# Kernel tuning notes

Hardware: AMD Instinct MI355X
Metric: run time of the kernel (lower is better)

Reference implementation:

```python
import jax, jax.numpy as jnp
import numpy as np

B, C_ATT, C_VAL = 1, 64, 64
T, H, W = 40, 32, 32
HW = H * W
TOPK = 10
TEMP = 0.07
NEIGHBOR_RANGE = 24  # circle mode -> radius = 24 // 2
NON_MASK_LEN = 1     # first frame is not masked
NEG_INF = -1e30


def _spatial_neighbor_circle(h, w, neighbor_range):
    """Circle-mode spatial neighbor mask, (h*w, h*w) bool."""
    radius = neighbor_range // 2
    gy, gx = jnp.meshgrid(jnp.arange(h, dtype=jnp.float32),
                          jnp.arange(w, dtype=jnp.float32), indexing='ij')
    dy = gy[:, :, None, None] - gy[None, None, :, :]
    dx = gx[:, :, None, None] - gx[None, None, :, :]
    dist = jnp.sqrt(dy * dy + dx * dx)
    return (dist < radius).reshape(h * w, h * w)


def setup_inputs() -> dict:
    key0 = jax.random.key(0)
    k1, k2, k3 = jax.random.split(key0, 3)
    query = jax.random.normal(k1, (B, C_ATT, H, W), dtype=jnp.float32)
    key = jax.random.normal(k2, (B, C_ATT, T, H, W), dtype=jnp.float32)
    value = jax.random.normal(k3, (B, C_VAL, T, H, W), dtype=jnp.float32)
    mask = _spatial_neighbor_circle(H, W, NEIGHBOR_RANGE)  # (HW, HW) bool
    return {"query": query, "key": key, "value": value, "mask": mask}


def _l2_normalize(x, axis, eps=1e-12):
    # matches F.normalize(p=2): x / max(||x||, eps)
    n = jnp.sqrt(jnp.sum(x * x, axis=axis, keepdims=True))
    return x / jnp.maximum(n, eps)


def reference(query, key, value, mask):
    # normalize along channel dim
    q = _l2_normalize(query, axis=1).reshape(B, C_ATT, HW)          # (B,C,Q)
    k = _l2_normalize(key, axis=1).reshape(B, C_ATT, T * HW)        # (B,C,K)
    v = value.reshape(B, C_VAL, T * HW)                             # (B,Cv,K)

    # affinity over all keys vs all queries (chunking in the original is a
    # pure memory optimization; the math per query column is identical)
    aff = jnp.einsum('bck,bcq->bkq', k, q) / TEMP                   # (B,K,Q)

    # build full mask: first NON_MASK_LEN frames fully visible, remaining
    # frames restricted to the spatial-neighbor circle
    tiled = jnp.tile(mask, (T - NON_MASK_LEN, 1))                   # ((T-nm)*HW, Q)
    full_mask = jnp.concatenate(
        [jnp.ones((NON_MASK_LEN * HW, HW), dtype=bool), tiled], axis=0)  # (K,Q)
    aff = jnp.where(full_mask[None], aff, NEG_INF)

    # top-k over the key dimension, per query
    aff_qk = jnp.swapaxes(aff, 1, 2)                                # (B,Q,K)
    top_vals, top_idx = jax.lax.top_k(aff_qk, TOPK)                 # (B,Q,topk)
    weights = jax.nn.softmax(top_vals, axis=-1)                     # (B,Q,topk)

    # gather top-k values: (B,Cv,Q,topk)
    gathered = jnp.take_along_axis(v[:, :, None, :], top_idx[:, None, :, :], axis=3)
    out = jnp.einsum('bcqk,bqk->bcq', gathered, weights)            # (B,Cv,Q)
    return out.reshape(B, C_VAL, H, W)
```

## Files before the change

### kernel.cpp

```cpp
#include <hip/hip_runtime.h>
#include <hip/hip_bf16.h>
#include <float.h>

#define HWQ   1024
#define NK    40960
#define NCH   64
#define NTOP  10
#define NJOBS 82
#define NPART (NJOBS * NTOP)
#define R2    144
#define CAP   48
#define TSCALE 14.2857142857142857f
#define LOSCL  4.8828125e-4f

typedef _Float16 f16x8 __attribute__((ext_vector_type(8)));
typedef float    f32x4 __attribute__((ext_vector_type(4)));
typedef unsigned long long u64;
typedef unsigned int       u32;

__device__ inline float bf16bits_to_f32(unsigned short u) {
    union { u32 i; float f; } z; z.i = ((u32)u) << 16; return z.f;
}
__device__ inline unsigned short f32_to_bf16bits(float x) {
    __hip_bfloat16 b = __float2bfloat16(x);
    return *(unsigned short*)&b;
}

__device__ inline int sniff_fp32(const unsigned short* __restrict__ raw) {
    const int lane = threadIdx.x & 63;
    const int e = (raw[lane] >> 7) & 0xFF;
    const u64 m = __ballot(e < 100 || e > 133);
    return __popcll(m) > 16;
}

__device__ inline u64 pack_vi(float val, int kidx) {
    const u32 b = __float_as_uint(val);
    const u32 u = b ^ (u32)(((int)b >> 31) | (int)0x80000000);
    return ((u64)u << 16) | (u32)(0xFFFF - kidx);
}
__device__ inline float unpack_val(u64 p) {
    const u32 u = (u32)(p >> 16);
    const u32 b = u ^ (~((u32)((int)u >> 31)) | 0x80000000u);
    return __uint_as_float(b);
}
__device__ inline int unpack_idx(u64 p) { return 0xFFFF - (int)(p & 0xFFFF); }

__device__ inline void ins10(u64* v, u64 pk) {
#pragma unroll
    for (int j = NTOP - 1; j >= 1; --j) {
        const bool gj = pk > v[j];
        const bool gp = pk > v[j - 1];
        v[j] = gj ? (gp ? v[j - 1] : pk) : v[j];
    }
    if (pk > v[0]) v[0] = pk;
}

__global__ __launch_bounds__(64) void prep_all(
    const void* __restrict__ qin_, const void* __restrict__ kin_,
    const void* __restrict__ vin_,
    f16x8* __restrict__ kh, f16x8* __restrict__ kl,
    f16x8* __restrict__ qh, f16x8* __restrict__ ql,
    unsigned short* __restrict__ vt)
{
    const int isf  = sniff_fp32((const unsigned short*)kin_);
    const int bid  = blockIdx.x;
    const int lane = threadIdx.x;

    if (bid < NK / 64) {
        const int key = bid * 64 + lane;
        float kv[NCH];
        if (isf) {
            const float* p = (const float*)kin_;
#pragma unroll
            for (int c = 0; c < NCH; ++c) kv[c] = p[c * NK + key];
        } else {
            const __hip_bfloat16* p = (const __hip_bfloat16*)kin_;
#pragma unroll
            for (int c = 0; c < NCH; ++c) kv[c] = __bfloat162float(p[c * NK + key]);
        }
        float s = 0.f;
#pragma unroll
        for (int c = 0; c < NCH; ++c) s = fmaf(kv[c], kv[c], s);
        const float rn = 1.0f / fmaxf(sqrtf(s), 1e-12f);

        const int tb = (key >> 4) * 128 + (key & 15);
#pragma unroll
        for (int blk = 0; blk < 8; ++blk) {
            f16x8 h, l;
#pragma unroll
            for (int j = 0; j < 8; ++j) {
                const float x = kv[blk * 8 + j] * rn;
                const _Float16 hh = (_Float16)x;
                h[j] = hh;
                l[j] = (_Float16)((x - (float)hh) * 2048.0f);
            }
            kh[tb + blk * 16] = h;
            kl[tb + blk * 16] = l;
        }

        if (isf) {
            const float* p = (const float*)vin_;
#pragma unroll
            for (int c = 0; c < NCH; ++c)
                vt[(size_t)key * NCH + c] = f32_to_bf16bits(p[c * NK + key]);
        } else {
            const unsigned short* p = (const unsigned short*)vin_;
#pragma unroll
            for (int c = 0; c < NCH; ++c) vt[(size_t)key * NCH + c] = p[c * NK + key];
        }
    } else {
        const int q = (bid - NK / 64) * 64 + lane;
        float qv[NCH];
        if (isf) {
            const float* p = (const float*)qin_;
#pragma unroll
            for (int c = 0; c < NCH; ++c) qv[c] = p[c * HWQ + q];
        } else {
            const __hip_bfloat16* p = (const __hip_bfloat16*)qin_;
#pragma unroll
            for (int c = 0; c < NCH; ++c) qv[c] = __bfloat162float(p[c * HWQ + q]);
        }
        float s = 0.f;
#pragma unroll
        for (int c = 0; c < NCH; ++c) s = fmaf(qv[c], qv[c], s);
        const float rn = 1.0f / fmaxf(sqrtf(s), 1e-12f);

        const int tb = (q >> 4) * 128 + (q & 15);
#pragma unroll
        for (int blk = 0; blk < 8; ++blk) {
            f16x8 h, l;
#pragma unroll
            for (int j = 0; j < 8; ++j) {
                const float x = qv[blk * 8 + j] * rn;
                const _Float16 hh = (_Float16)x;
                h[j] = hh;
                l[j] = (_Float16)((x - (float)hh) * 2048.0f);
            }
            qh[tb + blk * 16] = h;
            ql[tb + blk * 16] = l;
        }
    }
}

__device__ inline void quad_merge_store(
    u64 (*sm)[16][NTOP], int lane, u64* out10)
{
    int p0 = 0, p1 = 0, p2 = 0, p3 = 0;
#pragma unroll
    for (int r = 0; r < NTOP; ++r) {
        const u64 h0 = sm[0][lane][p0], h1 = sm[1][lane][p1];
        const u64 h2 = sm[2][lane][p2], h3 = sm[3][lane][p3];
        u64 m = h0; int sel = 0;
        if (h1 > m) { m = h1; sel = 1; }
        if (h2 > m) { m = h2; sel = 2; }
        if (h3 > m) { m = h3; sel = 3; }
        out10[r] = m;
        p0 += (sel == 0); p1 += (sel == 1); p2 += (sel == 2); p3 += (sel == 3);
    }
}

__global__ __launch_bounds__(128) void attn_f0(
    const f16x8* __restrict__ kh, const f16x8* __restrict__ kl,
    const f16x8* __restrict__ qh, const f16x8* __restrict__ ql,
    u64* __restrict__ pv, float* __restrict__ th)
{
    __shared__ u64 sm[2][4][16][NTOP];

    const int tid  = threadIdx.x;
    const int w    = tid >> 6;
    const int lane = tid & 63;
    const int quad = lane >> 4;
    const int n    = lane & 15;

    const int t   = blockIdx.x * 2 + w;
    const int job = blockIdx.y;

    const int qb = t * 128 + n;
    const f16x8 bh0 = qh[qb + (0 + quad) * 16];
    const f16x8 bh1 = qh[qb + (4 + quad) * 16];
    const f16x8 bl0 = ql[qb + (0 + quad) * 16];
    const f16x8 bl1 = ql[qb + (4 + quad) * 16];

    u64 v[NTOP];
#pragma unroll
    for (int j = 0; j < NTOP; ++j) v[j] = 0ull;

    const int start = job * 16, end = start + 16;
    int base = start * 128 + n;
    f16x8 nah0 = kh[base + (0 + quad) * 16], nah1 = kh[base + (4 + quad) * 16];
    f16x8 nal0 = kl[base + (0 + quad) * 16], nal1 = kl[base + (4 + quad) * 16];

    for (int kt = start; kt < end; ++kt) {
        const f16x8 ah0 = nah0, ah1 = nah1, al0 = nal0, al1 = nal1;
        const int ktn = (kt + 1 < end) ? kt + 1 : kt;
        base = ktn * 128 + n;
        nah0 = kh[base + (0 + quad) * 16]; nah1 = kh[base + (4 + quad) * 16];
        nal0 = kl[base + (0 + quad) * 16]; nal1 = kl[base + (4 + quad) * 16];

        f32x4 accH = {0.f,0.f,0.f,0.f}, accL0 = {0.f,0.f,0.f,0.f}, accL1 = {0.f,0.f,0.f,0.f};
        accH  = __builtin_amdgcn_mfma_f32_16x16x32_f16(ah0, bh0, accH, 0, 0, 0);
        accH  = __builtin_amdgcn_mfma_f32_16x16x32_f16(ah1, bh1, accH, 0, 0, 0);
        accL0 = __builtin_amdgcn_mfma_f32_16x16x32_f16(ah0, bl0, accL0, 0, 0, 0);
        accL0 = __builtin_amdgcn_mfma_f32_16x16x32_f16(al0, bh0, accL0, 0, 0, 0);
        accL1 = __builtin_amdgcn_mfma_f32_16x16x32_f16(ah1, bl1, accL1, 0, 0, 0);
        accL1 = __builtin_amdgcn_mfma_f32_16x16x32_f16(al1, bh1, accL1, 0, 0, 0);

        const int key0 = kt * 16 + quad * 4;
#pragma unroll
        for (int r = 0; r < 4; ++r) {
            const float val = fmaf(accL0[r] + accL1[r], LOSCL, accH[r]);
            const u64 pk = pack_vi(val, key0 + r);
            if (pk > v[NTOP - 1]) ins10(v, pk);
        }
    }

#pragma unroll
    for (int j = 0; j < NTOP; ++j) sm[w][quad][n][j] = v[j];
    __syncthreads();

    if (lane < 16) {
        u64 out10[NTOP];
        quad_merge_store(sm[w], lane, out10);
        const int q = t * 16 + lane;
#pragma unroll
        for (int r = 0; r < NTOP; ++r) pv[(size_t)q * NPART + job * NTOP + r] = out10[r];
        th[q * 4 + job] = unpack_val(out10[9]);
    }
}

__global__ __launch_bounds__(128) void attn_masked(
    const f16x8* __restrict__ kh, const f16x8* __restrict__ kl,
    const f16x8* __restrict__ qh, const f16x8* __restrict__ ql,
    const float* __restrict__ th, u64* __restrict__ pv)
{
    __shared__ u64 cand[2][16][CAP];
    __shared__ int cnt[2][16];

    const int tid  = threadIdx.x;
    const int w    = tid >> 6;
    const int lane = tid & 63;
    const int quad = lane >> 4;
    const int n    = lane & 15;

    const int qy   = blockIdx.x;
    const int t    = qy * 2 + w;
    const int yy   = blockIdx.y;
    const int f    = (yy >> 1) + 1;
    const int half = yy & 1;
    const int qx   = (t & 1) * 16 + n;
    const int q    = t * 16 + n;

    if (tid < 32) cnt[tid >> 4][tid & 15] = 0;
    __syncthreads();

    const float theta = fmaxf(fmaxf(th[q * 4 + 0], th[q * 4 + 1]),
                              fmaxf(th[q * 4 + 2], th[q * 4 + 3]));

    const int qb = t * 128 + n;
    const f16x8 bh0 = qh[qb + (0 + quad) * 16];
    const f16x8 bh1 = qh[qb + (4 + quad) * 16];
    const f16x8 bl0 = ql[qb + (0 + quad) * 16];
    const f16x8 bl1 = ql[qb + (4 + quad) * 16];

    const int rlo  = (qy > 11) ? qy - 11 : 0;
    const int rhi  = (qy < 20) ? qy + 11 : 31;
    const int mid  = (rlo + rhi + 1) >> 1;
    const int row0 = half ? mid : rlo;
    const int row1 = half ? rhi + 1 : mid;
    const int start = f * 64 + 2 * row0;
    const int end   = f * 64 + 2 * row1;

    int base = start * 128 + n;
    f16x8 nah0 = kh[base + (0 + quad) * 16], nah1 = kh[base + (4 + quad) * 16];
    f16x8 nal0 = kl[base + (0 + quad) * 16], nal1 = kl[base + (4 + quad) * 16];

    for (int kt = start; kt < end; ++kt) {
        const f16x8 ah0 = nah0, ah1 = nah1, al0 = nal0, al1 = nal1;
        const int ktn = (kt + 1 < end) ? kt + 1 : kt;
        base = ktn * 128 + n;
        nah0 = kh[base + (0 + quad) * 16]; nah1 = kh[base + (4 + quad) * 16];
        nal0 = kl[base + (0 + quad) * 16]; nal1 = kl[base + (4 + quad) * 16];

        f32x4 accH = {0.f,0.f,0.f,0.f}, accL0 = {0.f,0.f,0.f,0.f}, accL1 = {0.f,0.f,0.f,0.f};
        accH  = __builtin_amdgcn_mfma_f32_16x16x32_f16(ah0, bh0, accH, 0, 0, 0);
        accH  = __builtin_amdgcn_mfma_f32_16x16x32_f16(ah1, bh1, accH, 0, 0, 0);
        accL0 = __builtin_amdgcn_mfma_f32_16x16x32_f16(ah0, bl0, accL0, 0, 0, 0);
        accL0 = __builtin_amdgcn_mfma_f32_16x16x32_f16(al0, bh0, accL0, 0, 0, 0);
        accL1 = __builtin_amdgcn_mfma_f32_16x16x32_f16(ah1, bl1, accL1, 0, 0, 0);
        accL1 = __builtin_amdgcn_mfma_f32_16x16x32_f16(al1, bh1, accL1, 0, 0, 0);

        const int ky   = (kt >> 1) & 31;
        const int dy   = ky - qy;
        const int rem  = R2 - dy * dy;
        const int d0   = (kt & 1) * 16 + quad * 4 - qx;
        const int key0 = kt * 16 + quad * 4;
#pragma unroll
        for (int r = 0; r < 4; ++r) {
            const float val = fmaf(accL0[r] + accL1[r], LOSCL, accH[r]);
            const int dx = d0 + r;
            if (val > theta && dx * dx < rem) {
                const int pos = atomicAdd(&cnt[w][n], 1);
                if (pos < CAP) cand[w][n][pos] = pack_vi(val, key0 + r);
            }
        }
    }

    __syncthreads();
    if (lane < 16) {
        const int c = min(cnt[w][lane], CAP);
        u64 v[NTOP];
#pragma unroll
        for (int j = 0; j < NTOP; ++j) v[j] = 0ull;
        for (int e = 0; e < c; ++e) {
            const u64 pk = cand[w][lane][e];
            if (pk > v[NTOP - 1]) ins10(v, pk);
        }
        const int qq  = t * 16 + lane;
        const int job = 4 + (f - 1) * 2 + half;
#pragma unroll
        for (int r = 0; r < NTOP; ++r)
            pv[(size_t)qq * NPART + (size_t)job * NTOP + r] = v[r];
    }
}

__global__ __launch_bounds__(64) void finalize_kernel(
    const u64* __restrict__ pv, const unsigned short* __restrict__ vt,
    const unsigned short* __restrict__ kin_raw, void* __restrict__ out_)
{
    const int isf  = sniff_fp32(kin_raw);
    const int q    = blockIdx.x;
    const int lane = threadIdx.x;

    u64 lv[13];
#pragma unroll
    for (int e = 0; e < 13; ++e) {
        const int idx = e * 64 + lane;
        lv[e] = (idx < NPART) ? pv[(size_t)q * NPART + idx] : 0ull;
    }

    float wv[NTOP]; int wi[NTOP];
#pragma unroll
    for (int r = 0; r < NTOP; ++r) {
        u64 m = lv[0];
#pragma unroll
        for (int e = 1; e < 13; ++e) if (lv[e] > m) m = lv[e];
#pragma unroll
        for (int off = 32; off >= 1; off >>= 1) {
            const u32 lo = (u32)m, hi = (u32)(m >> 32);
            const u32 lo2 = (u32)__shfl_xor((int)lo, off);
            const u32 hi2 = (u32)__shfl_xor((int)hi, off);
            const u64 o = ((u64)hi2 << 32) | lo2;
            if (o > m) m = o;
        }
#pragma unroll
        for (int e = 0; e < 13; ++e) if (lv[e] == m) lv[e] = 0ull;
        wv[r] = unpack_val(m); wi[r] = unpack_idx(m);
    }

    float ww[NTOP]; float wsum = 0.f;
#pragma unroll
    for (int r = 0; r < NTOP; ++r) { ww[r] = expf((wv[r] - wv[0]) * TSCALE); wsum += ww[r]; }
    const float inv = 1.0f / wsum;

    float acc = 0.f;
#pragma unroll
    for (int r = 0; r < NTOP; ++r)
        acc += ww[r] * bf16bits_to_f32(vt[(size_t)wi[r] * NCH + lane]);
    const float res = acc * inv;

    if (isf) ((float*)out_)[lane * HWQ + q] = res;
    else     ((__hip_bfloat16*)out_)[lane * HWQ + q] = __float2bfloat16(res);
}

extern "C" void kernel_launch(void* const* d_in, const int* in_sizes, int n_in,
                              void* d_out, int out_size, void* d_ws, size_t ws_size,
                              hipStream_t stream)
{
    const void* qin = d_in[0];
    const void* kin = d_in[1];
    const void* vin = d_in[2];

    char* w = (char*)d_ws;
    f16x8*          kh  = (f16x8*)(w);
    f16x8*          kl  = (f16x8*)(w + 5242880);
    f16x8*          qhv = (f16x8*)(w + 10485760);
    f16x8*          qlv = (f16x8*)(w + 10616832);
    unsigned short* vt  = (unsigned short*)(w + 10747904);
    u64*            pv  = (u64*)(w + 15990784);
    float*          th  = (float*)(w + 22708224);

    prep_all<<<NK / 64 + HWQ / 64, 64, 0, stream>>>(qin, kin, vin, kh, kl, qhv, qlv, vt);
    attn_f0<<<dim3(32, 4), 128, 0, stream>>>(kh, kl, qhv, qlv, pv, th);
    attn_masked<<<dim3(32, 78), 128, 0, stream>>>(kh, kl, qhv, qlv, th, pv);
    finalize_kernel<<<HWQ, 64, 0, stream>>>(pv, vt, (const unsigned short*)kin, d_out);
}
```

Measured before the change: 150.0 us.

## Split attention work into finer jobs, deepen prefetch, vectorize value transpose stores

Doubles the number of partial top-k jobs: frame 0 is split into 8 jobs and each masked frame into 4 row ranges. This gives more blocks and better load balance, and the masked grid is linearized with a swizzled block index. The key-tile loads are now double-buffered two tiles ahead, and the transposed value writes in prep use 16-byte vector stores. In exchange, finalize must merge twice as many partials, and the candidate cap drops to 32, which could overflow and lose candidates.

After: 143.6 us. -4.2%, faster.

```diff
diff --git a/kernel.cpp b/kernel.cpp
--- a/kernel.cpp
+++ b/kernel.cpp
@@ -6,15 +6,16 @@
 #define NK    40960
 #define NCH   64
 #define NTOP  10
-#define NJOBS 82
+#define NJOBS 164
 #define NPART (NJOBS * NTOP)
 #define R2    144
-#define CAP   48
+#define CAP   32
 #define TSCALE 14.2857142857142857f
 #define LOSCL  4.8828125e-4f
 
 typedef _Float16 f16x8 __attribute__((ext_vector_type(8)));
 typedef float    f32x4 __attribute__((ext_vector_type(4)));
+typedef unsigned short us8 __attribute__((ext_vector_type(8)));
 typedef unsigned long long u64;
 typedef unsigned int       u32;
 
@@ -98,15 +99,23 @@
             kl[tb + blk * 16] = l;
         }
 
+        unsigned short vv[NCH];
         if (isf) {
             const float* p = (const float*)vin_;
 #pragma unroll
-            for (int c = 0; c < NCH; ++c)
-                vt[(size_t)key * NCH + c] = f32_to_bf16bits(p[c * NK + key]);
+            for (int c = 0; c < NCH; ++c) vv[c] = f32_to_bf16bits(p[c * NK + key]);
         } else {
             const unsigned short* p = (const unsigned short*)vin_;
 #pragma unroll
-            for (int c = 0; c < NCH; ++c) vt[(size_t)key * NCH + c] = p[c * NK + key];
+            for (int c = 0; c < NCH; ++c) vv[c] = p[c * NK + key];
+        }
+        us8* dst = (us8*)(vt + (size_t)key * NCH);
+#pragma unroll
+        for (int j = 0; j < 8; ++j) {
+            us8 o;
+#pragma unroll
+            for (int e = 0; e < 8; ++e) o[e] = vv[j * 8 + e];
+            dst[j] = o;
         }
     } else {
         const int q = (bid - NK / 64) * 64 + lane;
@@ -185,17 +194,22 @@
 #pragma unroll
     for (int j = 0; j < NTOP; ++j) v[j] = 0ull;
 
-    const int start = job * 16, end = start + 16;
-    int base = start * 128 + n;
-    f16x8 nah0 = kh[base + (0 + quad) * 16], nah1 = kh[base + (4 + quad) * 16];
-    f16x8 nal0 = kl[base + (0 + quad) * 16], nal1 = kl[base + (4 + quad) * 16];
+    const int start = job * 8, end = start + 8;
+
+    int ba = start * 128 + n;
+    f16x8 Ah0 = kh[ba + quad * 16], Ah1 = kh[ba + (4 + quad) * 16];
+    f16x8 Al0 = kl[ba + quad * 16], Al1 = kl[ba + (4 + quad) * 16];
+    int bb = (start + 1) * 128 + n;
+    f16x8 Bh0 = kh[bb + quad * 16], Bh1 = kh[bb + (4 + quad) * 16];
+    f16x8 Bl0 = kl[bb + quad * 16], Bl1 = kl[bb + (4 + quad) * 16];
 
     for (int kt = start; kt < end; ++kt) {
-        const f16x8 ah0 = nah0, ah1 = nah1, al0 = nal0, al1 = nal1;
-        const int ktn = (kt + 1 < end) ? kt + 1 : kt;
-        base = ktn * 128 + n;
-        nah0 = kh[base + (0 + quad) * 16]; nah1 = kh[base + (4 + quad) * 16];
-        nal0 = kl[base + (0 + quad) * 16]; nal1 = kl[base + (4 + quad) * 16];
+        const f16x8 ah0 = Ah0, ah1 = Ah1, al0 = Al0, al1 = Al1;
+        Ah0 = Bh0; Ah1 = Bh1; Al0 = Bl0; Al1 = Bl1;
+        const int ktn = (kt + 2 < end) ? kt + 2 : kt;
+        const int bn = ktn * 128 + n;
+        Bh0 = kh[bn + quad * 16]; Bh1 = kh[bn + (4 + quad) * 16];
+        Bl0 = kl[bn + quad * 16]; Bl1 = kl[bn + (4 + quad) * 16];
 
         f32x4 accH = {0.f,0.f,0.f,0.f}, accL0 = {0.f,0.f,0.f,0.f}, accL1 = {0.f,0.f,0.f,0.f};
         accH  = __builtin_amdgcn_mfma_f32_16x16x32_f16(ah0, bh0, accH, 0, 0, 0);
@@ -224,7 +238,7 @@
         const int q = t * 16 + lane;
 #pragma unroll
         for (int r = 0; r < NTOP; ++r) pv[(size_t)q * NPART + job * NTOP + r] = out10[r];
-        th[q * 4 + job] = unpack_val(out10[9]);
+        th[q * 8 + job] = unpack_val(out10[9]);
     }
 }
 
@@ -242,19 +256,24 @@
     const int quad = lane >> 4;
     const int n    = lane & 15;
 
-    const int qy   = blockIdx.x;
-    const int t    = qy * 2 + w;
-    const int yy   = blockIdx.y;
-    const int f    = (yy >> 1) + 1;
-    const int half = yy & 1;
-    const int qx   = (t & 1) * 16 + n;
-    const int q    = t * 16 + n;
+    const int lin   = blockIdx.x;
+    const int j     = (lin & 7) * 624 + (lin >> 3);
+    const int fm1   = j >> 7;
+    const int rr    = j & 127;
+    const int qy    = rr >> 2;
+    const int qr    = rr & 3;
+    const int frame = fm1 + 1;
+
+    const int t  = qy * 2 + w;
+    const int qx = (t & 1) * 16 + n;
+    const int q  = t * 16 + n;
 
     if (tid < 32) cnt[tid >> 4][tid & 15] = 0;
     __syncthreads();
 
-    const float theta = fmaxf(fmaxf(th[q * 4 + 0], th[q * 4 + 1]),
-                              fmaxf(th[q * 4 + 2], th[q * 4 + 3]));
+    float theta = th[q * 8 + 0];
+#pragma unroll
+    for (int e = 1; e < 8; ++e) theta = fmaxf(theta, th[q * 8 + e]);
 
     const int qb = t * 128 + n;
     const f16x8 bh0 = qh[qb + (0 + quad) * 16];
@@ -262,24 +281,28 @@
     const f16x8 bl0 = ql[qb + (0 + quad) * 16];
     const f16x8 bl1 = ql[qb + (4 + quad) * 16];
 
-    const int rlo  = (qy > 11) ? qy - 11 : 0;
-    const int rhi  = (qy < 20) ? qy + 11 : 31;
-    const int mid  = (rlo + rhi + 1) >> 1;
-    const int row0 = half ? mid : rlo;
-    const int row1 = half ? rhi + 1 : mid;
-    const int start = f * 64 + 2 * row0;
-    const int end   = f * 64 + 2 * row1;
-
-    int base = start * 128 + n;
-    f16x8 nah0 = kh[base + (0 + quad) * 16], nah1 = kh[base + (4 + quad) * 16];
-    f16x8 nal0 = kl[base + (0 + quad) * 16], nal1 = kl[base + (4 + quad) * 16];
+    const int rlo   = (qy > 11) ? qy - 11 : 0;
+    const int rhi   = (qy < 20) ? qy + 11 : 31;
+    const int nrows = rhi - rlo + 1;
+    const int r0    = rlo + (qr * nrows) / 4;
+    const int r1    = rlo + ((qr + 1) * nrows) / 4;
+    const int start = frame * 64 + 2 * r0;
+    const int end   = frame * 64 + 2 * r1;
+
+    int ba = start * 128 + n;
+    f16x8 Ah0 = kh[ba + quad * 16], Ah1 = kh[ba + (4 + quad) * 16];
+    f16x8 Al0 = kl[ba + quad * 16], Al1 = kl[ba + (4 + quad) * 16];
+    int bb = (start + 1) * 128 + n;
+    f16x8 Bh0 = kh[bb + quad * 16], Bh1 = kh[bb + (4 + quad) * 16];
+    f16x8 Bl0 = kl[bb + quad * 16], Bl1 = kl[bb + (4 + quad) * 16];
 
     for (int kt = start; kt < end; ++kt) {
-        const f16x8 ah0 = nah0, ah1 = nah1, al0 = nal0, al1 = nal1;
-        const int ktn = (kt + 1 < end) ? kt + 1 : kt;
-        base = ktn * 128 + n;
-        nah0 = kh[base + (0 + quad) * 16]; nah1 = kh[base + (4 + quad) * 16];
-        nal0 = kl[base + (0 + quad) * 16]; nal1 = kl[base + (4 + quad) * 16];
+        const f16x8 ah0 = Ah0, ah1 = Ah1, al0 = Al0, al1 = Al1;
+        Ah0 = Bh0; Ah1 = Bh1; Al0 = Bl0; Al1 = Bl1;
+        const int ktn = (kt + 2 < end) ? kt + 2 : kt;
+        const int bn = ktn * 128 + n;
+        Bh0 = kh[bn + quad * 16]; Bh1 = kh[bn + (4 + quad) * 16];
+        Bl0 = kl[bn + quad * 16]; Bl1 = kl[bn + (4 + quad) * 16];
 
         f32x4 accH = {0.f,0.f,0.f,0.f}, accL0 = {0.f,0.f,0.f,0.f}, accL1 = {0.f,0.f,0.f,0.f};
         accH  = __builtin_amdgcn_mfma_f32_16x16x32_f16(ah0, bh0, accH, 0, 0, 0);
@@ -310,13 +333,13 @@
         const int c = min(cnt[w][lane], CAP);
         u64 v[NTOP];
 #pragma unroll
-        for (int j = 0; j < NTOP; ++j) v[j] = 0ull;
+        for (int e = 0; e < NTOP; ++e) v[e] = 0ull;
         for (int e = 0; e < c; ++e) {
             const u64 pk = cand[w][lane][e];
             if (pk > v[NTOP - 1]) ins10(v, pk);
         }
         const int qq  = t * 16 + lane;
-        const int job = 4 + (f - 1) * 2 + half;
+        const int job = 8 + fm1 * 4 + qr;
 #pragma unroll
         for (int r = 0; r < NTOP; ++r)
             pv[(size_t)qq * NPART + (size_t)job * NTOP + r] = v[r];
@@ -331,9 +354,9 @@
     const int q    = blockIdx.x;
     const int lane = threadIdx.x;
 
-    u64 lv[13];
-#pragma unroll
-    for (int e = 0; e < 13; ++e) {
+    u64 lv[26];
+#pragma unroll
+    for (int e = 0; e < 26; ++e) {
         const int idx = e * 64 + lane;
         lv[e] = (idx < NPART) ? pv[(size_t)q * NPART + idx] : 0ull;
     }
@@ -343,7 +366,7 @@
     for (int r = 0; r < NTOP; ++r) {
         u64 m = lv[0];
 #pragma unroll
-        for (int e = 1; e < 13; ++e) if (lv[e] > m) m = lv[e];
+        for (int e = 1; e < 26; ++e) if (lv[e] > m) m = lv[e];
 #pragma unroll
         for (int off = 32; off >= 1; off >>= 1) {
             const u32 lo = (u32)m, hi = (u32)(m >> 32);
@@ -353,7 +376,7 @@
             if (o > m) m = o;
         }
 #pragma unroll
-        for (int e = 0; e < 13; ++e) if (lv[e] == m) lv[e] = 0ull;
+        for (int e = 0; e < 26; ++e) if (lv[e] == m) lv[e] = 0ull;
         wv[r] = unpack_val(m); wi[r] = unpack_idx(m);
     }
 
@@ -387,10 +410,10 @@
     f16x8*          qlv = (f16x8*)(w + 10616832);
     unsigned short* vt  = (unsigned short*)(w + 10747904);
     u64*            pv  = (u64*)(w + 15990784);
-    float*          th  = (float*)(w + 22708224);
+    float*          th  = (float*)(w + 29425664);
 
     prep_all<<<NK / 64 + HWQ / 64, 64, 0, stream>>>(qin, kin, vin, kh, kl, qhv, qlv, vt);
-    attn_f0<<<dim3(32, 4), 128, 0, stream>>>(kh, kl, qhv, qlv, pv, th);
-    attn_masked<<<dim3(32, 78), 128, 0, stream>>>(kh, kl, qhv, qlv, th, pv);
+    attn_f0<<<dim3(32, 8), 128, 0, stream>>>(kh, kl, qhv, qlv, pv, th);
+    attn_masked<<<4992, 128, 0, stream>>>(kh, kl, qhv, qlv, th, pv);
     finalize_kernel<<<HWQ, 64, 0, stream>>>(pv, vt, (const unsigned short*)kin, d_out);
 }
```
